# Optimization experiments

Hardware: AMD Instinct MI355X
Metric: run time of the kernel (lower is better)

Reference implementation:

```python
import jax, jax.numpy as jnp
import numpy as np

B, S, H = 4, 2048, 1024
DECAY_RATE = 0.5  # MemoryModule decay: exp(-decay_rate * k), k=1 (most recent pattern)


def setup_inputs() -> dict:
    key = jax.random.key(0)
    ks = jax.random.split(key, 7)
    hidden_states = jax.random.normal(ks[0], (B, S, H), dtype=jnp.float32)
    # past attention pattern: valid row-stochastic attention probs [B, S, S]
    pa = jax.random.uniform(ks[1], (B, S, S), dtype=jnp.float32)
    past_attention = pa / pa.sum(-1, keepdims=True)
    scale = 1.0 / np.sqrt(H).astype(np.float32)
    Wq = jax.random.normal(ks[2], (H, H), dtype=jnp.float32) * scale
    Wk = jax.random.normal(ks[3], (H, H), dtype=jnp.float32) * scale
    Wv = jax.random.normal(ks[4], (H, H), dtype=jnp.float32) * scale
    Wm = jax.random.normal(ks[5], (H, H), dtype=jnp.float32) * scale
    w_gate = jax.random.normal(ks[6], (H,), dtype=jnp.float32) * scale
    return {"hidden_states": hidden_states, "past_attention": past_attention,
            "Wq": Wq, "Wk": Wk, "Wv": Wv, "Wm": Wm, "w_gate": w_gate}


def reference(hidden_states, past_attention, Wq, Wk, Wv, Wm, w_gate):
    h = hidden_states.shape[-1]
    inv_sqrt_h = 1.0 / (h ** 0.5)
    # QKV projections (hidden -> hidden)
    q = jnp.einsum('bsh,hd->bsd', hidden_states, Wq)
    k = jnp.einsum('bsh,hd->bsd', hidden_states, Wk)
    v = jnp.einsum('bsh,hd->bsd', hidden_states, Wv)
    # base attention scores QK^T / sqrt(H)
    scores = jnp.einsum('bqd,bkd->bqk', q, k) * inv_sqrt_h
    # --- memory bias ---
    # decayed history pattern (single most-recent entry, k=1)
    memory = past_attention * jnp.exp(jnp.float32(-DECAY_RATE * 1.0))  # [B,S,S]
    # per-token scalar gate from query
    gates = jax.nn.sigmoid(jnp.einsum('bsh,h->bs', q, w_gate))  # [B,S]
    memory_values = jnp.einsum('bqk,bkd->bqd', memory, v)        # memory @ V
    transformed = jnp.einsum('bsh,hd->bsd', memory_values, Wm)   # memory_transform (no bias)
    gated_memory = gates[..., None] * transformed
    memory_bias = jnp.einsum('bqd,bkd->bqk', gated_memory, k) * inv_sqrt_h
    # augmented attention
    probs = jax.nn.softmax(scores + memory_bias, axis=-1)
    context = jnp.einsum('bqk,bkd->bqd', probs, v)
    return context
```

## Files before the change

### kernel.cpp

```cpp
#include <hip/hip_runtime.h>
#include <hip/hip_bf16.h>

typedef __attribute__((ext_vector_type(4))) float f32x4;
typedef __attribute__((ext_vector_type(8))) __bf16 bf16x8;

__device__ __forceinline__ unsigned short f2bf(float f) {
    union { float f; unsigned u; } x; x.f = f;
    unsigned r = x.u + 0x7fffu + ((x.u >> 16) & 1u);
    return (unsigned short)(r >> 16);
}
__device__ __forceinline__ float bf2f(unsigned short b) {
    union { unsigned u; float f; } x; x.u = ((unsigned)b) << 16;
    return x.f;
}

__device__ __forceinline__ void gload16(const void* g, void* l) {
    __builtin_amdgcn_global_load_lds(
        (const __attribute__((address_space(1))) unsigned int*)g,
        (__attribute__((address_space(3))) unsigned int*)l,
        16, 0, 0);
}

template <int N> __device__ __forceinline__ void vm_wait();
template <> __device__ __forceinline__ void vm_wait<0>() { asm volatile("s_waitcnt vmcnt(0)" ::: "memory"); }
template <> __device__ __forceinline__ void vm_wait<2>() { asm volatile("s_waitcnt vmcnt(2)" ::: "memory"); }
template <> __device__ __forceinline__ void vm_wait<4>() { asm volatile("s_waitcnt vmcnt(4)" ::: "memory"); }

__global__ __launch_bounds__(256) void k_wg2(const float* __restrict__ Wq,
                                             const float* __restrict__ wg,
                                             float* __restrict__ wg2) {
    int lane = threadIdx.x & 63;
    int row = blockIdx.x * 4 + (threadIdx.x >> 6);
    const float4* a = reinterpret_cast<const float4*>(Wq + (size_t)row * 1024);
    const float4* x = reinterpret_cast<const float4*>(wg);
    float s = 0.f;
    for (int i = lane; i < 256; i += 64) {
        float4 av = a[i], bv = x[i];
        s += av.x * bv.x + av.y * bv.y + av.z * bv.z + av.w * bv.w;
    }
#pragma unroll
    for (int o = 1; o < 64; o <<= 1) s += __shfl_xor(s, o);
    if (lane == 0) wg2[row] = s;
}

__global__ __launch_bounds__(256) void k_prep(
    const float* __restrict__ hs, const float* __restrict__ pa,
    const float* __restrict__ Wq, const float* __restrict__ Wk,
    const float* __restrict__ Wv, const float* __restrict__ Wm,
    unsigned short* __restrict__ hs_bf, unsigned short* __restrict__ pa_bf,
    unsigned short* __restrict__ WT, float decay,
    const float* __restrict__ wg2, float* __restrict__ gates) {
    __shared__ float tile[32][33];
    __shared__ float red[4];
    unsigned b = blockIdx.x;
    int t = threadIdx.x;
    if (b < 16384u) {
        int i = b * 256 + t;
        float4 v = reinterpret_cast<const float4*>(pa)[i];
        union { unsigned short u[4]; uint2 q; } o;
        o.u[0] = f2bf(v.x * decay); o.u[1] = f2bf(v.y * decay);
        o.u[2] = f2bf(v.z * decay); o.u[3] = f2bf(v.w * decay);
        reinterpret_cast<uint2*>(pa_bf)[i] = o.q;
    } else if (b < 24576u) {
        unsigned row = b - 16384u;
        int i = row * 256 + t;
        float4 v = reinterpret_cast<const float4*>(hs)[i];
        union { unsigned short u[4]; uint2 q; } o;
        o.u[0] = f2bf(v.x); o.u[1] = f2bf(v.y);
        o.u[2] = f2bf(v.z); o.u[3] = f2bf(v.w);
        reinterpret_cast<uint2*>(hs_bf)[i] = o.q;
        float4 w = reinterpret_cast<const float4*>(wg2)[t];
        float s = v.x * w.x + v.y * w.y + v.z * w.z + v.w * w.w;
#pragma unroll
        for (int o2 = 1; o2 < 64; o2 <<= 1) s += __shfl_xor(s, o2);
        if ((t & 63) == 0) red[t >> 6] = s;
        __syncthreads();
        if (t == 0) {
            float ss = red[0] + red[1] + red[2] + red[3];
            gates[row] = 1.f / (1.f + __expf(-ss));
        }
    } else {
        unsigned bb = b - 24576u;
        int z = bb >> 10, rem = bb & 1023;
        int bx = rem & 31, by = rem >> 5;
        const float* src = z == 0 ? Wq : z == 1 ? Wk : z == 2 ? Wv : Wm;
        unsigned short* dst = WT + (size_t)z * 1024 * 1024;
        int lx = t & 31, ly8 = t >> 5;
        int x = bx * 32 + lx;
#pragma unroll
        for (int i = 0; i < 4; i++)
            tile[ly8 + i * 8][lx] = src[(size_t)(by * 32 + ly8 + i * 8) * 1024 + x];
        __syncthreads();
        int tx = by * 32 + lx;
#pragma unroll
        for (int i = 0; i < 4; i++)
            dst[(size_t)(bx * 32 + ly8 + i * 8) * 1024 + tx] = f2bf(tile[lx][ly8 + i * 8]);
    }
}

__global__ __launch_bounds__(256) void k_post(const unsigned short* __restrict__ C3,
                                              unsigned short* __restrict__ v_t) {
    __shared__ unsigned short tile[32][33];
    unsigned b = blockIdx.x;
    int t = threadIdx.x;
    int bx = b & 31, by = (b >> 5) & 63, bz = b >> 11;
    int lx = t & 31, ly8 = t >> 5;
    int x = bx * 32 + lx;
#pragma unroll
    for (int i = 0; i < 4; i++) {
        int y = by * 32 + ly8 + i * 8;
        tile[ly8 + i * 8][lx] = C3[(size_t)(bz * 2048 + y) * 3072 + 2048 + x];
    }
    __syncthreads();
    int tx = by * 32 + lx;
#pragma unroll
    for (int i = 0; i < 4; i++) {
        int ty = bx * 32 + ly8 + i * 8;
        v_t[(size_t)bz * 1024 * 2048 + (size_t)ty * 2048 + tx] = tile[lx][ly8 + i * 8];
    }
}

template <int BN>
struct Geo {
    static constexpr int WN = BN / 64;
    static constexpr int WM = 8 / WN;
    static constexpr int WROWS = 256 / WM;
    static constexpr int MF = WROWS / 16;
    static constexpr int MP = MF / 4;
    static constexpr int ASZ = 256 * 64 * 2;
    static constexpr int BSZ = BN * 64 * 2;
    static constexpr int BUFSZ = ASZ + BSZ;
};

#define GPH(BUFOFF, MB, LB, STG, VMW)                                                   \
    {                                                                                   \
        const char* aB = smem + (BUFOFF);                                               \
        const char* bB = aB + G::ASZ;                                                   \
        bf16x8 af[G::MP * 2];                                                           \
        _Pragma("unroll") for (int mm = 0; mm < G::MP; ++mm)                            \
        _Pragma("unroll") for (int kk = 0; kk < 2; ++kk) {                              \
            int rowx = wrow + ((MB) + mm) * 16 + fr;                                    \
            int slot = (kk * 4 + kq) ^ (rowx & 7);                                      \
            af[mm * 2 + kk] = *reinterpret_cast<const bf16x8*>(aB + rowx * 128 + slot * 16); \
        }                                                                               \
        if (LB) {                                                                       \
            _Pragma("unroll") for (int nn = 0; nn < 4; ++nn)                            \
            _Pragma("unroll") for (int kk = 0; kk < 2; ++kk) {                          \
                int rowx = wcol + nn * 16 + fr;                                         \
                int slot = (kk * 4 + kq) ^ (rowx & 7);                                  \
                bfrag[nn * 2 + kk] = *reinterpret_cast<const bf16x8*>(bB + rowx * 128 + slot * 16); \
            }                                                                           \
        }                                                                               \
        STG;                                                                            \
        __builtin_amdgcn_sched_barrier(0);                                              \
        VMW;                                                                            \
        __builtin_amdgcn_s_barrier();                                                   \
        asm volatile("s_waitcnt lgkmcnt(0)" ::: "memory");                              \
        __builtin_amdgcn_sched_barrier(0);                                              \
        __builtin_amdgcn_s_setprio(1);                                                  \
        _Pragma("unroll") for (int mm = 0; mm < G::MP; ++mm)                            \
        _Pragma("unroll") for (int nn = 0; nn < 4; ++nn)                                \
        _Pragma("unroll") for (int kk = 0; kk < 2; ++kk)                                \
            acc[(MB) + mm][nn] = __builtin_amdgcn_mfma_f32_16x16x32_bf16(               \
                af[mm * 2 + kk], bfrag[nn * 2 + kk], acc[(MB) + mm][nn], 0, 0, 0);      \
        __builtin_amdgcn_s_setprio(0);                                                  \
        __builtin_amdgcn_sched_barrier(0);                                              \
        __builtin_amdgcn_s_barrier();                                                   \
        __builtin_amdgcn_sched_barrier(0);                                              \
    }

template <int EPI, int BN>
__device__ __forceinline__ void gemm_body(
    char* smem,
    const unsigned short* __restrict__ A, int ldA, long long bsA,
    const unsigned short* __restrict__ Bt, int ldB, long long bsB,
    void* __restrict__ Cv, int ldC, long long bsC,
    const unsigned short* __restrict__ Qm, int ldQ,
    const float* __restrict__ gates, float alpha, int K,
    int NX, int NY, int NB, int yf) {
    using G = Geo<BN>;
    const int NT = K >> 6, NI = K >> 7;

    unsigned b = blockIdx.x;
    unsigned wg = (b & 7) * (gridDim.x >> 3) + (b >> 3);
    int xT, yT, zB;
    if (yf) {
        yT = wg % NY; unsigned r2 = wg / NY;
        xT = r2 % NX; zB = (int)(r2 / NX) % NB;
    } else {
        xT = wg % NX; unsigned r2 = wg / NX;
        yT = r2 % NY; zB = (int)(r2 / NY) % NB;
    }

    const unsigned short* Ab = A + (size_t)zB * (size_t)bsA;
    const unsigned short* Bb = Bt + (size_t)zB * (size_t)bsB;

    int t = threadIdx.x, lane = t & 63, wave = t >> 6;
    int wc = wave % G::WN, wr = wave / G::WN;
    int fr = lane & 15, kq = lane >> 4;
    int wrow = wr * G::WROWS, wcol = wc * 64;
    int trow = t >> 3, csx = (t & 7) ^ (trow & 7);
    long long rowTile = (long long)yT * 256, colTile = (long long)xT * BN;

    f32x4 acc[G::MF][4];
#pragma unroll
    for (int m = 0; m < G::MF; ++m)
#pragma unroll
        for (int n = 0; n < 4; ++n) acc[m][n] = (f32x4){0.f, 0.f, 0.f, 0.f};
    bf16x8 bfrag[8];

    auto stageA = [&](int buf, int h, int tt) {
        int kt = tt < NT ? tt : NT - 1;
#pragma unroll
        for (int rr = 0; rr < 2; ++rr) {
            const unsigned short* src =
                Ab + (size_t)(rowTile + h * 128 + rr * 64 + trow) * (size_t)ldA + kt * 64 + csx * 8;
            gload16(src, smem + buf * G::BUFSZ + h * 16384 + rr * 8192 + t * 16);
        }
    };
    auto stageB = [&](int buf, int h, int tt) {
        int kt = tt < NT ? tt : NT - 1;
        if (BN == 256) {
#pragma unroll
            for (int rr = 0; rr < 2; ++rr) {
                const unsigned short* src =
                    Bb + (size_t)(colTile + h * 128 + rr * 64 + trow) * (size_t)ldB + kt * 64 + csx * 8;
                gload16(src, smem + buf * G::BUFSZ + G::ASZ + h * 16384 + rr * 8192 + t * 16);
            }
        } else {
            const unsigned short* src =
                Bb + (size_t)(colTile + h * 64 + trow) * (size_t)ldB + kt * 64 + csx * 8;
            gload16(src, smem + buf * G::BUFSZ + G::ASZ + h * 8192 + t * 16);
        }
    };

    stageA(0, 0, 0); stageA(0, 1, 0);
    stageB(0, 0, 0); stageB(0, 1, 0);
    stageB(1, 0, 1); stageB(1, 1, 1);
    __builtin_amdgcn_sched_barrier(0);
    vm_wait<0>();
    __builtin_amdgcn_s_barrier();
    __builtin_amdgcn_sched_barrier(0);

    constexpr int VMN = (BN == 256) ? 4 : 2;
    for (int i = 0; i < NI; ++i) {
        int t1 = 2 * i + 1, t2 = 2 * i + 2, t3 = 2 * i + 3;
        GPH(0,          0,         1, stageA(1, 0, t1), (void)0);
        GPH(0,          G::MP,     0, stageA(1, 1, t1), (void)0);
        GPH(0,          2 * G::MP, 0, stageB(0, 0, t2), (void)0);
        GPH(0,          3 * G::MP, 0, stageB(0, 1, t2), vm_wait<VMN>());
        GPH(G::BUFSZ,   0,         1, stageA(0, 0, t2), (void)0);
        GPH(G::BUFSZ,   G::MP,     0, stageA(0, 1, t2), (void)0);
        GPH(G::BUFSZ,   2 * G::MP, 0, stageB(1, 0, t3), (void)0);
        GPH(G::BUFSZ,   3 * G::MP, 0, stageB(1, 1, t3), vm_wait<VMN>());
    }
    vm_wait<0>();

    long long rb0 = rowTile + wrow + kq * 4;
    long long cb0 = colTile + wcol + fr;
    if (EPI == 0) {
        unsigned short* C = (unsigned short*)Cv + (size_t)zB * (size_t)bsC;
#pragma unroll
        for (int m = 0; m < G::MF; ++m)
#pragma unroll
            for (int n = 0; n < 4; ++n)
#pragma unroll
                for (int r = 0; r < 4; ++r)
                    C[(size_t)(rb0 + m * 16 + r) * (size_t)ldC + cb0 + n * 16] =
                        f2bf(acc[m][n][r] * alpha);
    } else if (EPI == 1) {
        unsigned short* C = (unsigned short*)Cv;
#pragma unroll
        for (int m = 0; m < G::MF; ++m)
#pragma unroll
            for (int r = 0; r < 4; ++r) {
                long long row = rb0 + m * 16 + r;
                float g = gates[row];
#pragma unroll
                for (int n = 0; n < 4; ++n) {
                    long long col = cb0 + n * 16;
                    float v = (bf2f(Qm[(size_t)row * (size_t)ldQ + col]) + g * acc[m][n][r]) * alpha;
                    C[(size_t)row * (size_t)ldC + col] = f2bf(v);
                }
            }
    } else if (EPI == 4) {
        float* C = (float*)Cv + (size_t)zB * (size_t)bsC;
#pragma unroll
        for (int m = 0; m < G::MF; ++m)
#pragma unroll
            for (int r = 0; r < 4; ++r) {
                long long row = rb0 + m * 16 + r;
                const float4* pp = reinterpret_cast<const float4*>(
                    gates + ((size_t)zB * 2048 + row) * 8);
                float4 p0 = pp[0], p1 = pp[1];
                float g = 1.f / (p0.x + p0.y + p0.z + p0.w + p1.x + p1.y + p1.z + p1.w);
#pragma unroll
                for (int n = 0; n < 4; ++n)
                    C[(size_t)row * (size_t)ldC + cb0 + n * 16] = acc[m][n][r] * g;
            }
    } else if (EPI == 5) {
        unsigned short* C = (unsigned short*)Cv + (size_t)zB * (size_t)bsC;
        float* partials = (float*)gates;
        float srow[G::MF][4];
#pragma unroll
        for (int m = 0; m < G::MF; ++m)
#pragma unroll
            for (int r = 0; r < 4; ++r) srow[m][r] = 0.f;
#pragma unroll
        for (int m = 0; m < G::MF; ++m)
#pragma unroll
            for (int n = 0; n < 4; ++n)
#pragma unroll
                for (int r = 0; r < 4; ++r) {
                    float e = __expf(acc[m][n][r] * alpha);
                    C[(size_t)(rb0 + m * 16 + r) * (size_t)ldC + cb0 + n * 16] = f2bf(e);
                    srow[m][r] += e;
                }
#pragma unroll
        for (int m = 0; m < G::MF; ++m)
#pragma unroll
            for (int r = 0; r < 4; ++r) {
#pragma unroll
                for (int msk = 1; msk < 16; msk <<= 1)
                    srow[m][r] += __shfl_xor(srow[m][r], msk);
            }
        float* sums = (float*)smem;
        if (fr == 0) {
#pragma unroll
            for (int m = 0; m < G::MF; ++m)
#pragma unroll
                for (int r = 0; r < 4; ++r)
                    sums[(wrow + kq * 4 + m * 16 + r) * G::WN + wc] = srow[m][r];
        }
        __syncthreads();
        if (t < 256) {
            float s = 0.f;
#pragma unroll
            for (int j = 0; j < G::WN; ++j) s += sums[t * G::WN + j];
            partials[((size_t)zB * 2048 + (size_t)rowTile + t) * 8 + xT] = s;
        }
    }
}

#define GEMM_ARGS                                                                     \
    const unsigned short *A, int ldA, long long bsA, const unsigned short *Bt,        \
        int ldB, long long bsB, void *Cv, int ldC, long long bsC,                     \
        const unsigned short *Qm, int ldQ, const float *gates, float alpha, int K,    \
        int NX, int NY, int NB, int yf
#define GEMM_PASS A, ldA, bsA, Bt, ldB, bsB, Cv, ldC, bsC, Qm, ldQ, gates, alpha, K, NX, NY, NB, yf

__global__ __launch_bounds__(512, 2) void k_qkv(GEMM_ARGS) {
    extern __shared__ char smem[];
    gemm_body<0, 128>(smem, GEMM_PASS);
}
__global__ __launch_bounds__(512, 2) void k_mv(GEMM_ARGS) {
    extern __shared__ char smem[];
    gemm_body<0, 128>(smem, GEMM_PASS);
}
__global__ __launch_bounds__(512, 2) void k_u(GEMM_ARGS) {
    extern __shared__ char smem[];
    gemm_body<1, 128>(smem, GEMM_PASS);
}
__global__ __launch_bounds__(512, 2) void k_logits(GEMM_ARGS) {
    extern __shared__ char smem[];
    gemm_body<5, 256>(smem, GEMM_PASS);
}
__global__ __launch_bounds__(512, 2) void k_ctx(GEMM_ARGS) {
    extern __shared__ char smem[];
    gemm_body<4, 128>(smem, GEMM_PASS);
}

extern "C" void kernel_launch(void* const* d_in, const int* in_sizes, int n_in,
                              void* d_out, int out_size, void* d_ws, size_t ws_size,
                              hipStream_t stream) {
    const float* hs = (const float*)d_in[0];
    const float* pa = (const float*)d_in[1];
    const float* Wq = (const float*)d_in[2];
    const float* Wk = (const float*)d_in[3];
    const float* Wv = (const float*)d_in[4];
    const float* Wm = (const float*)d_in[5];
    const float* wg = (const float*)d_in[6];
    float* out = (float*)d_out;

    const int B = 4, S = 2048, H = 1024;
    const size_t BS = (size_t)B * S;
    const size_t BSH = BS * H;
    const size_t BSS = (size_t)B * S * S;
    const float inv_sqrt_h = 0.03125f;
    const float decay = 0.60653065971263342f;

    char* ws = (char*)d_ws;
    size_t off = 0;
    auto take = [&](size_t bytes) {
        char* p = ws + off;
        off += (bytes + 255) & ~(size_t)255;
        return p;
    };
    unsigned short* hs_bf = (unsigned short*)take(BSH * 2);
    unsigned short* WT    = (unsigned short*)take(4ull * H * H * 2);
    float* wg2            = (float*)take(H * 4);
    float* gates          = (float*)take(BS * 4);
    unsigned short* C3    = (unsigned short*)take(BS * 3 * H * 2);
    unsigned short* v_t   = (unsigned short*)take(BSH * 2);
    unsigned short* pa_bf = (unsigned short*)take(BSS * 2);
    float* partials       = (float*)take(BS * 8 * 4);
    unsigned short* mv    = (unsigned short*)d_out;
    unsigned short* u_bf  = hs_bf;
    unsigned short* probs = pa_bf;
    unsigned short* WmT   = WT + 3ull * H * H;

    (void)hipFuncSetAttribute((const void*)k_qkv,    hipFuncAttributeMaxDynamicSharedMemorySize, 98304);
    (void)hipFuncSetAttribute((const void*)k_mv,     hipFuncAttributeMaxDynamicSharedMemorySize, 98304);
    (void)hipFuncSetAttribute((const void*)k_u,      hipFuncAttributeMaxDynamicSharedMemorySize, 98304);
    (void)hipFuncSetAttribute((const void*)k_ctx,    hipFuncAttributeMaxDynamicSharedMemorySize, 98304);
    (void)hipFuncSetAttribute((const void*)k_logits, hipFuncAttributeMaxDynamicSharedMemorySize, 131072);

    k_wg2<<<dim3(256), 256, 0, stream>>>(Wq, wg, wg2);
    k_prep<<<dim3(28672), 256, 0, stream>>>(hs, pa, Wq, Wk, Wv, Wm, hs_bf, pa_bf, WT, decay, wg2, gates);
    k_qkv<<<768, 512, 98304, stream>>>(
        hs_bf, H, 0, WT, H, 0, C3, 3 * H, 0, nullptr, 0, nullptr, 1.f, H, 24, 32, 1, 1);
    k_post<<<dim3(8192), 256, 0, stream>>>(C3, v_t);
    k_mv<<<256, 512, 98304, stream>>>(
        pa_bf, S, (long long)S * S, v_t, S, (long long)H * S, mv, H, (long long)S * H,
        nullptr, 0, nullptr, 1.f, S, 8, 8, 4, 1);
    k_u<<<256, 512, 98304, stream>>>(
        mv, H, 0, WmT, H, 0, u_bf, H, 0, C3, 3 * H, gates, inv_sqrt_h, H, 8, 32, 1, 1);
    k_logits<<<256, 512, 131072, stream>>>(
        u_bf, H, (long long)S * H, C3 + H, 3 * H, (long long)S * 3 * H,
        probs, S, (long long)S * S, nullptr, 0, partials, 1.f, H, 8, 8, 4, 1);
    k_ctx<<<256, 512, 98304, stream>>>(
        probs, S, (long long)S * S, v_t, S, (long long)H * S, out, H, (long long)S * H,
        nullptr, 0, partials, 1.f, S, 8, 8, 4, 1);
}
```

Measured before the change: 259.0 us.

## Compute V transposed directly via swapped GEMM, drop separate transpose kernel

Splits the fused QKV projection into a Q/K GEMM with wider 256-column tiles and a separate GEMM that computes V^T as WvT × hidden^T, writing v_t directly. The standalone k_post transpose kernel and the V third of the intermediate buffer are removed, along with their extra global memory read and write. The price is one more GEMM launch and a different tile shape and yf setting, so efficiency may shift. The new V^T GEMM uses batched stride arguments.

```diff
diff --git a/kernel.cpp b/kernel.cpp
--- a/kernel.cpp
+++ b/kernel.cpp
@@ -95,28 +95,6 @@
 #pragma unroll
         for (int i = 0; i < 4; i++)
             dst[(size_t)(bx * 32 + ly8 + i * 8) * 1024 + tx] = f2bf(tile[lx][ly8 + i * 8]);
-    }
-}
-
-__global__ __launch_bounds__(256) void k_post(const unsigned short* __restrict__ C3,
-                                              unsigned short* __restrict__ v_t) {
-    __shared__ unsigned short tile[32][33];
-    unsigned b = blockIdx.x;
-    int t = threadIdx.x;
-    int bx = b & 31, by = (b >> 5) & 63, bz = b >> 11;
-    int lx = t & 31, ly8 = t >> 5;
-    int x = bx * 32 + lx;
-#pragma unroll
-    for (int i = 0; i < 4; i++) {
-        int y = by * 32 + ly8 + i * 8;
-        tile[ly8 + i * 8][lx] = C3[(size_t)(bz * 2048 + y) * 3072 + 2048 + x];
-    }
-    __syncthreads();
-    int tx = by * 32 + lx;
-#pragma unroll
-    for (int i = 0; i < 4; i++) {
-        int ty = bx * 32 + ly8 + i * 8;
-        v_t[(size_t)bz * 1024 * 2048 + (size_t)ty * 2048 + tx] = tile[lx][ly8 + i * 8];
     }
 }
 
@@ -349,7 +327,11 @@
         int NX, int NY, int NB, int yf
 #define GEMM_PASS A, ldA, bsA, Bt, ldB, bsB, Cv, ldC, bsC, Qm, ldQ, gates, alpha, K, NX, NY, NB, yf
 
-__global__ __launch_bounds__(512, 2) void k_qkv(GEMM_ARGS) {
+__global__ __launch_bounds__(512, 2) void k_qk(GEMM_ARGS) {
+    extern __shared__ char smem[];
+    gemm_body<0, 256>(smem, GEMM_PASS);
+}
+__global__ __launch_bounds__(512, 2) void k_vt(GEMM_ARGS) {
     extern __shared__ char smem[];
     gemm_body<0, 128>(smem, GEMM_PASS);
 }
@@ -400,16 +382,18 @@
     unsigned short* WT    = (unsigned short*)take(4ull * H * H * 2);
     float* wg2            = (float*)take(H * 4);
     float* gates          = (float*)take(BS * 4);
-    unsigned short* C3    = (unsigned short*)take(BS * 3 * H * 2);
+    unsigned short* C2    = (unsigned short*)take(BS * 2 * H * 2);
     unsigned short* v_t   = (unsigned short*)take(BSH * 2);
     unsigned short* pa_bf = (unsigned short*)take(BSS * 2);
     float* partials       = (float*)take(BS * 8 * 4);
     unsigned short* mv    = (unsigned short*)d_out;
     unsigned short* u_bf  = hs_bf;
     unsigned short* probs = pa_bf;
+    unsigned short* WvT   = WT + 2ull * H * H;
     unsigned short* WmT   = WT + 3ull * H * H;
 
-    (void)hipFuncSetAttribute((const void*)k_qkv,    hipFuncAttributeMaxDynamicSharedMemorySize, 98304);
+    (void)hipFuncSetAttribute((const void*)k_qk,     hipFuncAttributeMaxDynamicSharedMemorySize, 131072);
+    (void)hipFuncSetAttribute((const void*)k_vt,     hipFuncAttributeMaxDynamicSharedMemorySize, 98304);
     (void)hipFuncSetAttribute((const void*)k_mv,     hipFuncAttributeMaxDynamicSharedMemorySize, 98304);
     (void)hipFuncSetAttribute((const void*)k_u,      hipFuncAttributeMaxDynamicSharedMemorySize, 98304);
     (void)hipFuncSetAttribute((const void*)k_ctx,    hipFuncAttributeMaxDynamicSharedMemorySize, 98304);
@@ -417,16 +401,18 @@
 
     k_wg2<<<dim3(256), 256, 0, stream>>>(Wq, wg, wg2);
     k_prep<<<dim3(28672), 256, 0, stream>>>(hs, pa, Wq, Wk, Wv, Wm, hs_bf, pa_bf, WT, decay, wg2, gates);
-    k_qkv<<<768, 512, 98304, stream>>>(
-        hs_bf, H, 0, WT, H, 0, C3, 3 * H, 0, nullptr, 0, nullptr, 1.f, H, 24, 32, 1, 1);
-    k_post<<<dim3(8192), 256, 0, stream>>>(C3, v_t);
+    k_qk<<<256, 512, 131072, stream>>>(
+        hs_bf, H, 0, WT, H, 0, C2, 2 * H, 0, nullptr, 0, nullptr, 1.f, H, 8, 32, 1, 0);
+    k_vt<<<256, 512, 98304, stream>>>(
+        WvT, H, 0, hs_bf, H, (long long)S * H, v_t, S, (long long)H * S,
+        nullptr, 0, nullptr, 1.f, H, 16, 4, 4, 0);
     k_mv<<<256, 512, 98304, stream>>>(
         pa_bf, S, (long long)S * S, v_t, S, (long long)H * S, mv, H, (long long)S * H,
         nullptr, 0, nullptr, 1.f, S, 8, 8, 4, 1);
     k_u<<<256, 512, 98304, stream>>>(
-        mv, H, 0, WmT, H, 0, u_bf, H, 0, C3, 3 * H, gates, inv_sqrt_h, H, 8, 32, 1, 1);
+        mv, H, 0, WmT, H, 0, u_bf, H, 0, C2, 2 * H, gates, inv_sqrt_h, H, 8, 32, 1, 0);
     k_logits<<<256, 512, 131072, stream>>>(
-        u_bf, H, (long long)S * H, C3 + H, 3 * H, (long long)S * 3 * H,
+        u_bf, H, (long long)S * H, C2 + H, 2 * H, (long long)S * 2 * H,
         probs, S, (long long)S * S, nullptr, 0, partials, 1.f, H, 8, 8, 4, 1);
     k_ctx<<<256, 512, 98304, stream>>>(
         probs, S, (long long)S * S, v_t, S, (long long)H * S, out, H, (long long)S * H,
```

New measurement: 231.4 us (median of 2 runs). 10.6% less time.
